# Kernel tuning notes

Measured on AMD Instinct MI355X. Metric: run time of the kernel, lower is better.

The kernel has to match this reference:

```python
import jax, jax.numpy as jnp
import numpy as np

B, L, C = 64, 2048, 20
H1, H2, F = 384, 16, 20


def _gru(x, h0, Wih, Whh, bih, bhh):
    """PyTorch-semantics GRU, batch_first. x:(B,L,I), h0:(B,H) -> (ys:(B,L,H), hT:(B,H))."""
    H = h0.shape[-1]
    # Precompute all input projections at once: (B, L, 3H)
    xp = jnp.einsum('bli,gi->blg', x, Wih) + bih

    def step(h, xp_t):
        gh = h @ Whh.T + bhh  # (B, 3H)
        r = jax.nn.sigmoid(xp_t[:, :H] + gh[:, :H])
        z = jax.nn.sigmoid(xp_t[:, H:2 * H] + gh[:, H:2 * H])
        n = jnp.tanh(xp_t[:, 2 * H:] + r * gh[:, 2 * H:])
        h_new = (1.0 - z) * n + z * h
        return h_new, h_new

    hT, ys = jax.lax.scan(step, h0, jnp.swapaxes(xp, 0, 1))
    return jnp.swapaxes(ys, 0, 1), hT


def _init_gru(key, I, H):
    k1, k2, k3, k4 = jax.random.split(key, 4)
    s = 1.0 / np.sqrt(H)
    return (jax.random.uniform(k1, (3 * H, I), minval=-s, maxval=s),
            jax.random.uniform(k2, (3 * H, H), minval=-s, maxval=s),
            jax.random.uniform(k3, (3 * H,), minval=-s, maxval=s),
            jax.random.uniform(k4, (3 * H,), minval=-s, maxval=s))


def setup_inputs() -> dict:
    key = jax.random.key(0)
    ks = jax.random.split(key, 6)
    x = jax.random.normal(ks[0], (B, L, C), dtype=jnp.float32)
    Wih1, Whh1, bih1, bhh1 = _init_gru(ks[1], C, H1)
    Wih2, Whh2, bih2, bhh2 = _init_gru(ks[2], H1, H2)
    Wih3, Whh3, bih3, bhh3 = _init_gru(ks[3], F, F)
    s = 1.0 / np.sqrt(H2)
    Wfc = jax.random.uniform(ks[4], (F, H2), minval=-s, maxval=s)
    bfc = jax.random.uniform(ks[5], (F,), minval=-s, maxval=s)
    return {
        'x': x,
        'h1': jnp.zeros((B, H1), jnp.float32),
        'h2': jnp.zeros((B, H2), jnp.float32),
        'h3': jnp.zeros((B, F), jnp.float32),
        'Wih1': Wih1, 'Whh1': Whh1, 'bih1': bih1, 'bhh1': bhh1,
        'Wih2': Wih2, 'Whh2': Whh2, 'bih2': bih2, 'bhh2': bhh2,
        'Wih3': Wih3, 'Whh3': Whh3, 'bih3': bih3, 'bhh3': bhh3,
        'Wfc': Wfc, 'bfc': bfc,
    }


def reference(x, h1, h2, h3,
              Wih1, Whh1, bih1, bhh1,
              Wih2, Whh2, bih2, bhh2,
              Wih3, Whh3, bih3, bhh3,
              Wfc, bfc):
    y1, h1f = _gru(x, h1, Wih1, Whh1, bih1, bhh1)          # (B, L, 384)
    y2, h2f = _gru(y1, h2, Wih2, Whh2, bih2, bhh2)         # (B, L, 16)
    y2 = jax.nn.relu(y2)
    # cat of two identical copies -> dual_fc -> sum over copy dim == 2 * tanh(fc)
    x_mid = 2.0 * jnp.tanh(jnp.einsum('blh,fh->blf', y2, Wfc) + bfc)  # (B, L, 20)
    y3, h3f = _gru(jnp.flip(x_mid, axis=1), h3, Wih3, Whh3, bih3, bhh3)
    x_out = jnp.tanh(y3)                                    # (B, L, 20)
    return (x_mid, x_out, h1f, h2f, h3f)
```

## Files before the change

### kernel.cpp

```cpp
#include <hip/hip_runtime.h>

typedef _Float16 f16x8 __attribute__((ext_vector_type(8)));
typedef _Float16 f16x2 __attribute__((ext_vector_type(2)));

union F16x8U { f16x8 v8; f16x2 v2[4]; };
union FP16U { _Float16 h; unsigned short u; };

__device__ __forceinline__ float dot2acc(f16x2 a, f16x2 b, float c) {
#if __has_builtin(__builtin_amdgcn_fdot2)
    return __builtin_amdgcn_fdot2(a, b, c, false);
#else
    return c + (float)a[0] * (float)b[0] + (float)a[1] * (float)b[1];
#endif
}

__device__ __forceinline__ float sigmoidf_(float x) {
    return __builtin_amdgcn_rcpf(1.f + __expf(-x));
}

__device__ __forceinline__ float tanhf_(float x) {
    float a = fabsf(x);
    float e = __expf(-2.f * a);
    float r = (1.f - e) * __builtin_amdgcn_rcpf(1.f + e);
    return copysignf(r, x);
}


__global__ void pack_weights(const float* __restrict__ Whh1,
                             const float* __restrict__ Wih1,
                             const float* __restrict__ Wih2,
                             _Float16* __restrict__ wsbase) {
    int tid = blockIdx.x * 256 + threadIdx.x;
    f16x8* whhp  = (f16x8*)wsbase;
    f16x8* wih1p = (f16x8*)(wsbase + 442368);
    _Float16* wih2h = wsbase + 470016;
    if (tid < 55296) {
        int c = tid % 18, thr = tid / 18;
        int g = c / 6, m = c % 6;
        int jl = thr % 96, ko = (thr / 96) % 8, q = thr / 768;
        int row = g * 384 + q * 96 + jl;
        int kb = ko * 48 + m * 8;
        f16x8 v;
#pragma unroll
        for (int i = 0; i < 8; ++i) v[i] = (_Float16)Whh1[row * 384 + kb + i];
        whhp[tid] = v;
    } else if (tid < 58752) {
        int t2 = tid - 55296;
        int m = t2 % 3, thr = t2 / 3;
        int jl = thr % 96, g = (thr / 96) % 3, q = thr / 288;
        int row = g * 384 + q * 96 + jl;
        f16x8 v;
#pragma unroll
        for (int i = 0; i < 8; ++i) {
            int kk = m * 8 + i;
            v[i] = (kk < 20) ? (_Float16)Wih1[row * 20 + kk] : (_Float16)0.f;
        }
        wih1p[t2] = v;
    } else if (tid < 77184) {
        int t3 = tid - 58752;
        wih2h[t3] = (_Float16)Wih2[t3];
    }
}

__global__ __launch_bounds__(768, 3) void gru1_scan(
    const float* __restrict__ x, const float* __restrict__ h1_0,
    const float* __restrict__ bih1, const float* __restrict__ bhh1,
    const f16x8* __restrict__ whhp, const f16x8* __restrict__ wih1p,
    const _Float16* __restrict__ wih2h,
    float* __restrict__ sxp2g, unsigned* __restrict__ exch,
    float* __restrict__ h1f_o) {
    const int bid = blockIdx.x;
    const int b = bid >> 2, q = bid & 3;
    const int tid = threadIdx.x;
    const int ko = tid / 96, jl = tid % 96;

    __shared__ __align__(16) _Float16 h1h[384];
    __shared__ __align__(16) _Float16 hhist[4][384];
    __shared__ __align__(16) _Float16 xsh[2][24];
    __shared__ __align__(16) float4 part4[8 * 96];
    __shared__ float part2[4 * 12 * 65];

    F16x8U W[18];
    {
        const f16x8* wp = whhp + ((size_t)((q * 8 + ko) * 96 + jl)) * 18;
#pragma unroll
        for (int c = 0; c < 18; ++c) W[c].v8 = wp[c];
    }
    F16x8U Wx[3];
    if (ko < 3) {
        const f16x8* wp = wih1p + ((size_t)((q * 3 + ko) * 96 + jl)) * 3;
#pragma unroll
        for (int c = 0; c < 3; ++c) Wx[c].v8 = wp[c];
    }

    float cbr = 0.f, cbz = 0.f, cxn = 0.f, chn = 0.f, hprev = 0.f;
    if (tid < 96) {
        int j = q * 96 + tid;
        cbr = bih1[j] + bhh1[j];
        cbz = bih1[384 + j] + bhh1[384 + j];
        cxn = bih1[768 + j];
        chn = bhh1[768 + j];
        hprev = h1_0[b * 384 + j];
    }
    if (tid < 384) h1h[tid] = (_Float16)h1_0[b * 384 + tid];
    const float* xb = x + (size_t)b * 40960;
    if (tid < 24) {
        xsh[0][tid] = (_Float16)((tid < 20) ? xb[tid] : 0.f);
        xsh[1][tid] = (_Float16)0.f;
    }

    unsigned* exb0 = exch + (size_t)b * 384;
    unsigned* exb1 = exch + 24576 + (size_t)b * 384;
    const int rs = tid - 384;
    const int gslot = (rs >= 0 && rs < 288) ? ((q * 96 + 96 + rs) % 384) : 0;

    const int o2 = tid >> 6, ks = tid & 63;
    const _Float16* w2row = wih2h + (q * 12 + o2) * 384 + ks * 6;

    __syncthreads();

    for (int t = 0; t < 2048; ++t) {
        float ar = 0.f, az = 0.f, ahn = 0.f, axn = 0.f;
        const _Float16* hbase = h1h + ko * 48;
#pragma unroll
        for (int m = 0; m < 6; ++m) {
            F16x8U hv; hv.v8 = *(const f16x8*)(hbase + m * 8);
#pragma unroll
            for (int i = 0; i < 4; ++i) {
                ar  = dot2acc(W[m].v2[i],      hv.v2[i], ar);
                az  = dot2acc(W[6 + m].v2[i],  hv.v2[i], az);
                ahn = dot2acc(W[12 + m].v2[i], hv.v2[i], ahn);
            }
        }
        if (ko < 3) {
            float acc = 0.f;
            const _Float16* xs = xsh[t & 1];
#pragma unroll
            for (int m = 0; m < 3; ++m) {
                F16x8U xv; xv.v8 = *(const f16x8*)(xs + m * 8);
#pragma unroll
                for (int i = 0; i < 4; ++i)
                    acc = dot2acc(Wx[m].v2[i], xv.v2[i], acc);
            }
            if (ko == 0) ar += acc;
            else if (ko == 1) az += acc;
            else axn += acc;
        }
        part4[ko * 96 + jl] = make_float4(ar, az, ahn, axn);
        __syncthreads();

        const unsigned tag = (unsigned)(t + 1);
        unsigned* exw = ((t + 1) & 1) ? exb1 : exb0;
        if (tid < 96) {
            float sr = cbr, sz = cbz, snh = chn, snx = cxn;
#pragma unroll
            for (int k = 0; k < 8; ++k) {
                float4 p = part4[k * 96 + tid];
                sr += p.x; sz += p.y; snh += p.z; snx += p.w;
            }
            float r = sigmoidf_(sr), z = sigmoidf_(sz);
            float n = tanhf_(snx + r * snh);
            hprev = (1.f - z) * n + z * hprev;
            FP16U hu; hu.h = (_Float16)hprev;
            __hip_atomic_store(&exw[q * 96 + tid], (tag << 16) | (unsigned)hu.u,
                               __ATOMIC_RELAXED, __HIP_MEMORY_SCOPE_AGENT);
            h1h[q * 96 + tid] = hu.h;
            hhist[t & 3][q * 96 + tid] = hu.h;
        }
        if (tid >= 96 && tid < 116 && t + 1 < 2048)
            xsh[(t + 1) & 1][tid - 96] = (_Float16)xb[(t + 1) * 20 + (tid - 96)];
        if (tid >= 384 && tid < 672) {
            unsigned w;
            do {
                w = __hip_atomic_load(&exw[gslot], __ATOMIC_RELAXED,
                                      __HIP_MEMORY_SCOPE_AGENT);
            } while ((w >> 16) != tag);
            FP16U hu; hu.u = (unsigned short)(w & 0xffffu);
            h1h[gslot] = hu.h;
            hhist[t & 3][gslot] = hu.h;
        }
        __syncthreads();

        if ((t & 3) == 3) {
            f16x2 w0 = *(const f16x2*)(w2row);
            f16x2 w1 = *(const f16x2*)(w2row + 2);
            f16x2 w2 = *(const f16x2*)(w2row + 4);
#pragma unroll
            for (int tq = 0; tq < 4; ++tq) {
                const _Float16* hrow = hhist[tq] + ks * 6;
                float a = dot2acc(w0, *(const f16x2*)hrow, 0.f);
                a = dot2acc(w1, *(const f16x2*)(hrow + 2), a);
                a = dot2acc(w2, *(const f16x2*)(hrow + 4), a);
                part2[(tq * 12 + o2) * 65 + ks] = a;
            }
            __syncthreads();
            if (tid < 48) {
                int tq = tid / 12, o = tid % 12;
                const float* pr = &part2[(tq * 12 + o) * 65];
                float s0 = 0.f, s1 = 0.f, s2 = 0.f, s3 = 0.f;
#pragma unroll
                for (int i2 = 0; i2 < 16; ++i2) {
                    s0 += pr[i2 * 4];     s1 += pr[i2 * 4 + 1];
                    s2 += pr[i2 * 4 + 2]; s3 += pr[i2 * 4 + 3];
                }
                __hip_atomic_store(
                    &sxp2g[((size_t)b * 2048 + (t - 3 + tq)) * 48 + q * 12 + o],
                    (s0 + s1) + (s2 + s3), __ATOMIC_RELAXED,
                    __HIP_MEMORY_SCOPE_AGENT);
            }
        }
    }
    if (tid < 96) h1f_o[b * 384 + q * 96 + tid] = hprev;
}

__global__ __launch_bounds__(64) void tail_scan(
    const float* __restrict__ sxp2g, const float* __restrict__ h2_0,
    const float* __restrict__ h3_0,
    const float* __restrict__ Whh2, const float* __restrict__ bih2,
    const float* __restrict__ bhh2,
    const float* __restrict__ Wfc, const float* __restrict__ bfc,
    const float* __restrict__ Wih3, const float* __restrict__ Whh3,
    const float* __restrict__ bih3, const float* __restrict__ bhh3,
    float* __restrict__ xmid, float* __restrict__ xout,
    float* __restrict__ h2f_o, float* __restrict__ h3f_o) {
    const int b = blockIdx.x;
    const int l = threadIdx.x;

    __shared__ __align__(16) float hs[32];

    float w2r[16]; float bx2 = 0.f, bh2 = 0.f;
    if (l < 48) {
#pragma unroll
        for (int k = 0; k < 16; ++k) w2r[k] = Whh2[l * 16 + k];
        bx2 = bih2[l]; bh2 = bhh2[l];
    }
    float wfc[16]; float bf = 0.f;
    if (l < 20) {
#pragma unroll
        for (int k = 0; k < 16; ++k) wfc[k] = Wfc[l * 16 + k];
        bf = bfc[l];
    }
    float h2all[16];
    {
        const float4* hp = (const float4*)(h2_0 + b * 16);
#pragma unroll
        for (int c = 0; c < 4; ++c) {
            float4 v = hp[c];
            h2all[c * 4 + 0] = v.x; h2all[c * 4 + 1] = v.y;
            h2all[c * 4 + 2] = v.z; h2all[c * 4 + 3] = v.w;
        }
    }
    float hown = (l < 16) ? h2_0[b * 16 + l] : 0.f;

    float* xm = xmid + (size_t)b * 40960;
    const float* sx = sxp2g + (size_t)b * 98304;

    float pre[8];
#pragma unroll
    for (int i = 0; i < 8; ++i) pre[i] = (l < 48) ? sx[i * 48 + l] : 0.f;

    for (int tg = 0; tg < 256; ++tg) {
#pragma unroll
        for (int tq = 0; tq < 8; ++tq) {
            const int t = tg * 8 + tq;
            float ax = pre[tq] + bx2;
            if (l < 48 && t + 8 < 2048) pre[tq] = sx[(size_t)(t + 8) * 48 + l];
            float a0 = 0.f, a1 = 0.f;
#pragma unroll
            for (int k = 0; k < 8; ++k) {
                a0 = __builtin_fmaf(h2all[k], w2r[k], a0);
                a1 = __builtin_fmaf(h2all[8 + k], w2r[8 + k], a1);
            }
            float ah = bh2 + a0 + a1;
            float s_   = ax + ah;
            float zpre = __shfl(s_, (16 + l) & 63);
            float xn3  = __shfl(ax, (32 + l) & 63);
            float ghn  = __shfl(ah, (32 + l) & 63);
            float r2 = sigmoidf_(s_);
            float z2 = sigmoidf_(zpre);
            float n2 = tanhf_(xn3 + r2 * ghn);
            float h2n = (1.f - z2) * n2 + z2 * hown;
            if (l < 16) { hown = h2n; hs[l] = h2n; }
            __builtin_amdgcn_wave_barrier();
            {
                const float4* hv = (const float4*)hs;
#pragma unroll
                for (int c = 0; c < 4; ++c) {
                    float4 v = hv[c];
                    h2all[c * 4 + 0] = v.x; h2all[c * 4 + 1] = v.y;
                    h2all[c * 4 + 2] = v.z; h2all[c * 4 + 3] = v.w;
                }
            }
            float f0 = 0.f, f1 = 0.f;
#pragma unroll
            for (int k = 0; k < 8; ++k) {
                f0 = __builtin_fmaf(fmaxf(h2all[k], 0.f), wfc[k], f0);
                f1 = __builtin_fmaf(fmaxf(h2all[8 + k], 0.f), wfc[8 + k], f1);
            }
            float a = bf + f0 + f1;
            if (l < 20) xm[t * 20 + l] = 2.f * tanhf_(a);
        }
    }
    if (l < 16) h2f_o[b * 16 + l] = hown;

    float wi3[20], wh3[20]; float bx3 = 0.f, bh3 = 0.f;
    if (l < 60) {
#pragma unroll
        for (int k = 0; k < 20; ++k) {
            wi3[k] = Wih3[l * 20 + k];
            wh3[k] = Whh3[l * 20 + k];
        }
        bx3 = bih3[l]; bh3 = bhh3[l];
    }
    float h3all[20];
    {
        const float4* hp = (const float4*)(h3_0 + b * 20);
#pragma unroll
        for (int c = 0; c < 5; ++c) {
            float4 v = hp[c];
            h3all[c * 4 + 0] = v.x; h3all[c * 4 + 1] = v.y;
            h3all[c * 4 + 2] = v.z; h3all[c * 4 + 3] = v.w;
        }
    }
    float h3own = (l < 20) ? h3_0[b * 20 + l] : 0.f;
    float* xo = xout + (size_t)b * 40960;

    float4 px[4][5];
#pragma unroll
    for (int i = 0; i < 4; ++i) {
        const float4* xr = (const float4*)(xm + (size_t)(2047 - i) * 20);
#pragma unroll
        for (int c = 0; c < 5; ++c) px[i][c] = xr[c];
    }

    for (int tg = 0; tg < 512; ++tg) {
#pragma unroll
        for (int tq = 0; tq < 4; ++tq) {
            const int t = 2047 - (tg * 4 + tq);
            float xv[20];
#pragma unroll
            for (int c = 0; c < 5; ++c) {
                float4 v = px[tq][c];
                xv[c * 4 + 0] = v.x; xv[c * 4 + 1] = v.y;
                xv[c * 4 + 2] = v.z; xv[c * 4 + 3] = v.w;
            }
            if (t - 4 >= 0) {
                const float4* xr = (const float4*)(xm + (size_t)(t - 4) * 20);
#pragma unroll
                for (int c = 0; c < 5; ++c) px[tq][c] = xr[c];
            }
            float x0 = 0.f, x1 = 0.f, g0 = 0.f, g1 = 0.f;
#pragma unroll
            for (int k = 0; k < 10; ++k) {
                x0 = __builtin_fmaf(xv[k], wi3[k], x0);
                x1 = __builtin_fmaf(xv[10 + k], wi3[10 + k], x1);
                g0 = __builtin_fmaf(h3all[k], wh3[k], g0);
                g1 = __builtin_fmaf(h3all[10 + k], wh3[10 + k], g1);
            }
            float ax = bx3 + x0 + x1;
            float ah = bh3 + g0 + g1;
            float s_   = ax + ah;
            float zpre = __shfl(s_, (20 + l) & 63);
            float xn_  = __shfl(ax, (40 + l) & 63);
            float ghn  = __shfl(ah, (40 + l) & 63);
            float r = sigmoidf_(s_);
            float z = sigmoidf_(zpre);
            float n = tanhf_(xn_ + r * ghn);
            float hn = (1.f - z) * n + z * h3own;
            if (l < 20) {
                h3own = hn;
                hs[l] = hn;
                xo[(size_t)(2047 - t) * 20 + l] = tanhf_(hn);
            }
            __builtin_amdgcn_wave_barrier();
#pragma unroll
            for (int c = 0; c < 5; ++c) {
                float4 v = ((const float4*)hs)[c];
                h3all[c * 4 + 0] = v.x; h3all[c * 4 + 1] = v.y;
                h3all[c * 4 + 2] = v.z; h3all[c * 4 + 3] = v.w;
            }
        }
    }
    if (l < 20) h3f_o[b * 20 + l] = h3own;
}

extern "C" void kernel_launch(void* const* d_in, const int* in_sizes, int n_in,
                              void* d_out, int out_size, void* d_ws, size_t ws_size,
                              hipStream_t stream) {
    const float* x    = (const float*)d_in[0];
    const float* h1   = (const float*)d_in[1];
    const float* h2   = (const float*)d_in[2];
    const float* h3   = (const float*)d_in[3];
    const float* Wih1 = (const float*)d_in[4];
    const float* Whh1 = (const float*)d_in[5];
    const float* bih1 = (const float*)d_in[6];
    const float* bhh1 = (const float*)d_in[7];
    const float* Wih2 = (const float*)d_in[8];
    const float* Whh2 = (const float*)d_in[9];
    const float* bih2 = (const float*)d_in[10];
    const float* bhh2 = (const float*)d_in[11];
    const float* Wih3 = (const float*)d_in[12];
    const float* Whh3 = (const float*)d_in[13];
    const float* bih3 = (const float*)d_in[14];
    const float* bhh3 = (const float*)d_in[15];
    const float* Wfc  = (const float*)d_in[16];
    const float* bfc  = (const float*)d_in[17];

    float* out  = (float*)d_out;
    float* xmid = out;
    float* xout = out + 2621440;
    float* h1f  = out + 5242880;
    float* h2f  = out + 5267456;
    float* h3f  = out + 5268480;

    char* ws = (char*)d_ws;
    _Float16* wsh  = (_Float16*)ws;
    float*    sxp2 = (float*)(ws + 1048576);
    unsigned* exch = (unsigned*)(ws + 26214400);

    hipMemsetAsync(exch, 0, 196608, stream);
    pack_weights<<<302, 256, 0, stream>>>(Whh1, Wih1, Wih2, wsh);
    gru1_scan<<<256, 768, 0, stream>>>(x, h1, bih1, bhh1,
                                       (const f16x8*)wsh,
                                       (const f16x8*)(wsh + 442368),
                                       wsh + 470016,
                                       sxp2, exch, h1f);
    tail_scan<<<64, 64, 0, stream>>>(sxp2, h2, h3,
                                     Whh2, bih2, bhh2, Wfc, bfc,
                                     Wih3, Whh3, bih3, bhh3,
                                     xmid, xout, h2f, h3f);
}
```

Baseline: 5.059 ms.

## Batch 16 sequences per block and compute GRU1 recurrence with MFMA

After: 8.240 ms. 1.63x slower.

```diff
diff --git a/kernel.cpp b/kernel.cpp
--- a/kernel.cpp
+++ b/kernel.cpp
@@ -1,18 +1,11 @@
 #include <hip/hip_runtime.h>
 
 typedef _Float16 f16x8 __attribute__((ext_vector_type(8)));
-typedef _Float16 f16x2 __attribute__((ext_vector_type(2)));
-
-union F16x8U { f16x8 v8; f16x2 v2[4]; };
+typedef _Float16 f16x4 __attribute__((ext_vector_type(4)));
+typedef float f32x4 __attribute__((ext_vector_type(4)));
+typedef unsigned long long u64_t;
+
 union FP16U { _Float16 h; unsigned short u; };
-
-__device__ __forceinline__ float dot2acc(f16x2 a, f16x2 b, float c) {
-#if __has_builtin(__builtin_amdgcn_fdot2)
-    return __builtin_amdgcn_fdot2(a, b, c, false);
-#else
-    return c + (float)a[0] * (float)b[0] + (float)a[1] * (float)b[1];
-#endif
-}
 
 __device__ __forceinline__ float sigmoidf_(float x) {
     return __builtin_amdgcn_rcpf(1.f + __expf(-x));
@@ -25,192 +18,258 @@
     return copysignf(r, x);
 }
 
+__device__ __forceinline__ f32x4 mfma16(f16x8 a, f16x8 b, f32x4 c) {
+    return __builtin_amdgcn_mfma_f32_16x16x32_f16(a, b, c, 0, 0, 0);
+}
+
 
 __global__ void pack_weights(const float* __restrict__ Whh1,
                              const float* __restrict__ Wih1,
                              const float* __restrict__ Wih2,
                              _Float16* __restrict__ wsbase) {
     int tid = blockIdx.x * 256 + threadIdx.x;
-    f16x8* whhp  = (f16x8*)wsbase;
-    f16x8* wih1p = (f16x8*)(wsbase + 442368);
-    _Float16* wih2h = wsbase + 470016;
-    if (tid < 55296) {
-        int c = tid % 18, thr = tid / 18;
-        int g = c / 6, m = c % 6;
-        int jl = thr % 96, ko = (thr / 96) % 8, q = thr / 768;
-        int row = g * 384 + q * 96 + jl;
-        int kb = ko * 48 + m * 8;
+    f16x8* whhA  = (f16x8*)wsbase;
+    f16x8* wih2f = (f16x8*)(wsbase + 491520);
+    if (tid < 61440) {
+        int l = tid & 63, fr = tid >> 6;
+        int fslot = fr % 20, w = fr / 20;
+        int kh = w & 1, jq = w >> 1;
+        int jc = jq % 6, q = jq / 6;
+        int tile, kt;
+        if (kh == 0) {
+            if (fslot < 7)       { tile = 0; kt = fslot; }
+            else if (fslot < 14) { tile = 1; kt = fslot - 7; }
+            else                 { tile = 2; kt = fslot - 14; }
+        } else {
+            if (fslot < 6)       { tile = 0; kt = 7 + fslot; }
+            else if (fslot < 12) { tile = 1; kt = 1 + fslot; }
+            else if (fslot < 18) { tile = 2; kt = fslot - 6; }
+            else if (fslot == 18){ tile = 3; kt = 12; }
+            else                 { tile = 4; kt = 0; }
+        }
+        int gate = (tile == 0) ? 0 : (tile == 1) ? 1 : 2;
+        int row = gate * 384 + q * 96 + jc * 16 + (l & 15);
+        int k0 = kt * 32 + (l >> 4) * 8;
         f16x8 v;
 #pragma unroll
-        for (int i = 0; i < 8; ++i) v[i] = (_Float16)Whh1[row * 384 + kb + i];
-        whhp[tid] = v;
-    } else if (tid < 58752) {
-        int t2 = tid - 55296;
-        int m = t2 % 3, thr = t2 / 3;
-        int jl = thr % 96, g = (thr / 96) % 3, q = thr / 288;
-        int row = g * 384 + q * 96 + jl;
+        for (int i = 0; i < 8; ++i) {
+            float f = 0.f;
+            if (tile != 4) {
+                int k = k0 + i;
+                if (tile == 3) {
+                    int kx = k - 384;
+                    f = (kx < 20) ? Wih1[row * 20 + kx] : 0.f;
+                } else if (k < 384) {
+                    f = Whh1[row * 384 + k];
+                } else if (tile < 2) {
+                    int kx = k - 384;
+                    f = (kx < 20) ? Wih1[row * 20 + kx] : 0.f;
+                }
+            }
+            v[i] = (_Float16)f;
+        }
+        whhA[tid] = v;
+    } else if (tid < 63744) {
+        int t2 = tid - 61440;
+        int l = t2 & 63, fi = t2 >> 6;
+        int q = fi / 9, vv = fi % 9;
+        int Mt = vv / 3, kk = 3 * q + vv % 3;
+        int row = Mt * 16 + (l & 15);
+        int k0 = kk * 32 + (l >> 4) * 8;
         f16x8 v;
 #pragma unroll
-        for (int i = 0; i < 8; ++i) {
-            int kk = m * 8 + i;
-            v[i] = (kk < 20) ? (_Float16)Wih1[row * 20 + kk] : (_Float16)0.f;
-        }
-        wih1p[t2] = v;
-    } else if (tid < 77184) {
-        int t3 = tid - 58752;
-        wih2h[t3] = (_Float16)Wih2[t3];
-    }
-}
-
-__global__ __launch_bounds__(768, 3) void gru1_scan(
+        for (int i = 0; i < 8; ++i) v[i] = (_Float16)Wih2[row * 384 + k0 + i];
+        wih2f[t2] = v;
+    }
+}
+
+__global__ __launch_bounds__(768) void gru1_scan(
     const float* __restrict__ x, const float* __restrict__ h1_0,
     const float* __restrict__ bih1, const float* __restrict__ bhh1,
-    const f16x8* __restrict__ whhp, const f16x8* __restrict__ wih1p,
-    const _Float16* __restrict__ wih2h,
-    float* __restrict__ sxp2g, unsigned* __restrict__ exch,
+    const f16x8* __restrict__ whhA, const f16x8* __restrict__ wih2f,
+    float* __restrict__ sxp2g, u64_t* __restrict__ exch,
     float* __restrict__ h1f_o) {
     const int bid = blockIdx.x;
-    const int b = bid >> 2, q = bid & 3;
+    const int g = bid >> 2, q = bid & 3;
     const int tid = threadIdx.x;
-    const int ko = tid / 96, jl = tid % 96;
-
-    __shared__ __align__(16) _Float16 h1h[384];
-    __shared__ __align__(16) _Float16 hhist[4][384];
-    __shared__ __align__(16) _Float16 xsh[2][24];
-    __shared__ __align__(16) float4 part4[8 * 96];
-    __shared__ float part2[4 * 12 * 65];
-
-    F16x8U W[18];
+    const int v = tid >> 6, l = tid & 63;
+    const int jc = v >> 1, kh = v & 1;
+    const int rg = l >> 4, b = l & 15;
+    const int j0 = q * 96 + jc * 16 + rg * 4;
+
+    __shared__ __align__(16) _Float16 hbuf[2][6784];
+    __shared__ __align__(16) float part[6528];
+
+    f16x8 A[20];
     {
-        const f16x8* wp = whhp + ((size_t)((q * 8 + ko) * 96 + jl)) * 18;
-#pragma unroll
-        for (int c = 0; c < 18; ++c) W[c].v8 = wp[c];
-    }
-    F16x8U Wx[3];
-    if (ko < 3) {
-        const f16x8* wp = wih1p + ((size_t)((q * 3 + ko) * 96 + jl)) * 3;
-#pragma unroll
-        for (int c = 0; c < 3; ++c) Wx[c].v8 = wp[c];
-    }
-
-    float cbr = 0.f, cbz = 0.f, cxn = 0.f, chn = 0.f, hprev = 0.f;
-    if (tid < 96) {
-        int j = q * 96 + tid;
-        cbr = bih1[j] + bhh1[j];
-        cbz = bih1[384 + j] + bhh1[384 + j];
-        cxn = bih1[768 + j];
-        chn = bhh1[768 + j];
-        hprev = h1_0[b * 384 + j];
-    }
-    if (tid < 384) h1h[tid] = (_Float16)h1_0[b * 384 + tid];
-    const float* xb = x + (size_t)b * 40960;
-    if (tid < 24) {
-        xsh[0][tid] = (_Float16)((tid < 20) ? xb[tid] : 0.f);
-        xsh[1][tid] = (_Float16)0.f;
-    }
-
-    unsigned* exb0 = exch + (size_t)b * 384;
-    unsigned* exb1 = exch + 24576 + (size_t)b * 384;
-    const int rs = tid - 384;
-    const int gslot = (rs >= 0 && rs < 288) ? ((q * 96 + 96 + rs) % 384) : 0;
-
-    const int o2 = tid >> 6, ks = tid & 63;
-    const _Float16* w2row = wih2h + (q * 12 + o2) * 384 + ks * 6;
-
+        const f16x8* ap = whhA + (size_t)(((q * 6 + jc) * 2 + kh) * 20) * 64 + l;
+#pragma unroll
+        for (int c = 0; c < 20; ++c) A[c] = ap[c * 64];
+    }
+    const bool xw = (v < 9);
+    const int ktx = 3 * q + v % 3, Mtx = v / 3;
+    f16x8 Ax;
+    if (xw) Ax = wih2f[(q * 9 + v) * 64 + l];
+
+    float bR[4], bZ[4], bXN[4], bHN[4], hp[4];
+    if (kh == 0) {
+#pragma unroll
+        for (int i = 0; i < 4; ++i) {
+            int j = j0 + i;
+            bR[i]  = bih1[j] + bhh1[j];
+            bZ[i]  = bih1[384 + j] + bhh1[384 + j];
+            bXN[i] = bih1[768 + j];
+            bHN[i] = bhh1[768 + j];
+            hp[i]  = h1_0[(size_t)(g * 16 + b) * 384 + j];
+        }
+    }
+
+    int wo[6], lo[6];
+    const int p = jc * 64 + l;
+    if (kh == 1) {
+#pragma unroll
+        for (int k = 0; k < 6; ++k) {
+            int idx = p + 384 * k;
+            int r_ = idx >> 4, b2 = idx & 15;
+            int jwr = (q * 48 + 48 + r_) % 192;
+            wo[k] = jwr * 16 + b2;
+            lo[k] = b2 * 424 + jwr * 2;
+        }
+    }
+    const int bx_ = p / 20, xi_ = p % 20;
+
+    for (int idx = tid; idx < 6784; idx += 768) {
+        int bb = idx / 424, k = idx % 424;
+        float val = 0.f;
+        if (k < 384) val = h1_0[(size_t)(g * 16 + bb) * 384 + k];
+        else if (k < 404) val = x[(size_t)(g * 16 + bb) * 40960 + (k - 384)];
+        hbuf[0][idx] = (_Float16)val;
+        hbuf[1][idx] = (_Float16)0.f;
+    }
+    u64_t* exg = exch + (size_t)g * 6144;
     __syncthreads();
 
     for (int t = 0; t < 2048; ++t) {
-        float ar = 0.f, az = 0.f, ahn = 0.f, axn = 0.f;
-        const _Float16* hbase = h1h + ko * 48;
-#pragma unroll
-        for (int m = 0; m < 6; ++m) {
-            F16x8U hv; hv.v8 = *(const f16x8*)(hbase + m * 8);
+        const int cur = t & 1, nxt = cur ^ 1;
+        const _Float16* hc = hbuf[cur];
+        _Float16* hn = hbuf[nxt];
+        const unsigned tag = (unsigned)(t + 1);
+        u64_t* exw = exg + ((t + 1) & 1) * 3072;
+
+        float xreg = 0.f;
+        if (kh == 1 && p < 320 && t + 1 < 2048)
+            xreg = x[(size_t)(g * 16 + bx_) * 40960 + (t + 1) * 20 + xi_];
+
+        f32x4 aR{0.f, 0.f, 0.f, 0.f}, aZ{0.f, 0.f, 0.f, 0.f};
+        f32x4 aN{0.f, 0.f, 0.f, 0.f}, aX{0.f, 0.f, 0.f, 0.f};
+        if (kh == 0) {
+#pragma unroll
+            for (int ki = 0; ki < 7; ++ki) {
+                f16x8 Bf = *(const f16x8*)(hc + b * 424 + ki * 32 + rg * 8);
+                aR = mfma16(A[ki], Bf, aR);
+                aZ = mfma16(A[7 + ki], Bf, aZ);
+                if (ki < 6) aN = mfma16(A[14 + ki], Bf, aN);
+            }
+        } else {
+#pragma unroll
+            for (int ki = 0; ki < 7; ++ki) {
+                f16x8 Bf = *(const f16x8*)(hc + b * 424 + (6 + ki) * 32 + rg * 8);
+                if (ki > 0) {
+                    aR = mfma16(A[ki - 1], Bf, aR);
+                    aZ = mfma16(A[5 + ki], Bf, aZ);
+                }
+                if (ki < 6) aN = mfma16(A[12 + ki], Bf, aN);
+                if (ki == 6) aX = mfma16(A[18], Bf, aX);
+            }
+        }
+
+        if (xw && t > 0) {
+            f16x8 Bx = *(const f16x8*)(hc + b * 424 + ktx * 32 + rg * 8);
+            f32x4 px = mfma16(Ax, Bx, (f32x4){0.f, 0.f, 0.f, 0.f});
+            float* dst = sxp2g + ((size_t)(g * 16 + b) * 2048 + (t - 1)) * 48 +
+                         Mtx * 16 + rg * 4;
+#pragma unroll
+            for (int i = 0; i < 4; ++i) atomicAdd(dst + i, px[i]);
+        }
+
+        if (kh == 1) {
+            float* pp = part + (jc * 64 + l) * 17;
 #pragma unroll
             for (int i = 0; i < 4; ++i) {
-                ar  = dot2acc(W[m].v2[i],      hv.v2[i], ar);
-                az  = dot2acc(W[6 + m].v2[i],  hv.v2[i], az);
-                ahn = dot2acc(W[12 + m].v2[i], hv.v2[i], ahn);
-            }
-        }
-        if (ko < 3) {
-            float acc = 0.f;
-            const _Float16* xs = xsh[t & 1];
-#pragma unroll
-            for (int m = 0; m < 3; ++m) {
-                F16x8U xv; xv.v8 = *(const f16x8*)(xs + m * 8);
-#pragma unroll
-                for (int i = 0; i < 4; ++i)
-                    acc = dot2acc(Wx[m].v2[i], xv.v2[i], acc);
-            }
-            if (ko == 0) ar += acc;
-            else if (ko == 1) az += acc;
-            else axn += acc;
-        }
-        part4[ko * 96 + jl] = make_float4(ar, az, ahn, axn);
+                pp[i] = aR[i]; pp[4 + i] = aZ[i];
+                pp[8 + i] = aN[i]; pp[12 + i] = aX[i];
+            }
+        }
         __syncthreads();
 
-        const unsigned tag = (unsigned)(t + 1);
-        unsigned* exw = ((t + 1) & 1) ? exb1 : exb0;
-        if (tid < 96) {
-            float sr = cbr, sz = cbz, snh = chn, snx = cxn;
-#pragma unroll
-            for (int k = 0; k < 8; ++k) {
-                float4 p = part4[k * 96 + tid];
-                sr += p.x; sz += p.y; snh += p.z; snx += p.w;
-            }
-            float r = sigmoidf_(sr), z = sigmoidf_(sz);
-            float n = tanhf_(snx + r * snh);
-            hprev = (1.f - z) * n + z * hprev;
-            FP16U hu; hu.h = (_Float16)hprev;
-            __hip_atomic_store(&exw[q * 96 + tid], (tag << 16) | (unsigned)hu.u,
-                               __ATOMIC_RELAXED, __HIP_MEMORY_SCOPE_AGENT);
-            h1h[q * 96 + tid] = hu.h;
-            hhist[t & 3][q * 96 + tid] = hu.h;
-        }
-        if (tid >= 96 && tid < 116 && t + 1 < 2048)
-            xsh[(t + 1) & 1][tid - 96] = (_Float16)xb[(t + 1) * 20 + (tid - 96)];
-        if (tid >= 384 && tid < 672) {
-            unsigned w;
+        if (kh == 0) {
+            const float* pp = part + (jc * 64 + l) * 17;
+            _Float16 hh[4];
+#pragma unroll
+            for (int i = 0; i < 4; ++i) {
+                float sR = aR[i] + pp[i];
+                float sZ = aZ[i] + pp[4 + i];
+                float sN = aN[i] + pp[8 + i];
+                float sX = aX[i] + pp[12 + i];
+                float r = sigmoidf_(sR + bR[i]);
+                float z = sigmoidf_(sZ + bZ[i]);
+                float n = tanhf_(sX + bXN[i] + r * (sN + bHN[i]));
+                float h = n + z * (hp[i] - n);
+                hp[i] = h;
+                hh[i] = (_Float16)h;
+            }
+            FP16U u0, u1, u2, u3;
+            u0.h = hh[0]; u1.h = hh[1]; u2.h = hh[2]; u3.h = hh[3];
+            unsigned w01 = (unsigned)u0.u | ((unsigned)u1.u << 16);
+            unsigned w23 = (unsigned)u2.u | ((unsigned)u3.u << 16);
+            u64_t e0 = (u64_t)w01 | ((u64_t)tag << 32);
+            u64_t e1 = (u64_t)w23 | ((u64_t)tag << 32);
+            int wA = (j0 >> 1) * 16 + b;
+            __hip_atomic_store(exw + wA, e0, __ATOMIC_RELAXED,
+                               __HIP_MEMORY_SCOPE_AGENT);
+            __hip_atomic_store(exw + wA + 16, e1, __ATOMIC_RELAXED,
+                               __HIP_MEMORY_SCOPE_AGENT);
+            f16x4 hq; hq[0] = hh[0]; hq[1] = hh[1]; hq[2] = hh[2]; hq[3] = hh[3];
+            *(f16x4*)(hn + b * 424 + j0) = hq;
+        } else {
+            if (p < 320 && t + 1 < 2048)
+                hn[bx_ * 424 + 384 + xi_] = (_Float16)xreg;
+            u64_t vv0, vv1, vv2, vv3, vv4, vv5;
+            bool ok;
             do {
-                w = __hip_atomic_load(&exw[gslot], __ATOMIC_RELAXED,
-                                      __HIP_MEMORY_SCOPE_AGENT);
-            } while ((w >> 16) != tag);
-            FP16U hu; hu.u = (unsigned short)(w & 0xffffu);
-            h1h[gslot] = hu.h;
-            hhist[t & 3][gslot] = hu.h;
+                vv0 = __hip_atomic_load(exw + wo[0], __ATOMIC_RELAXED, __HIP_MEMORY_SCOPE_AGENT);
+                vv1 = __hip_atomic_load(exw + wo[1], __ATOMIC_RELAXED, __HIP_MEMORY_SCOPE_AGENT);
+                vv2 = __hip_atomic_load(exw + wo[2], __ATOMIC_RELAXED, __HIP_MEMORY_SCOPE_AGENT);
+                vv3 = __hip_atomic_load(exw + wo[3], __ATOMIC_RELAXED, __HIP_MEMORY_SCOPE_AGENT);
+                vv4 = __hip_atomic_load(exw + wo[4], __ATOMIC_RELAXED, __HIP_MEMORY_SCOPE_AGENT);
+                vv5 = __hip_atomic_load(exw + wo[5], __ATOMIC_RELAXED, __HIP_MEMORY_SCOPE_AGENT);
+                ok = ((unsigned)(vv0 >> 32) == tag) & ((unsigned)(vv1 >> 32) == tag) &
+                     ((unsigned)(vv2 >> 32) == tag) & ((unsigned)(vv3 >> 32) == tag) &
+                     ((unsigned)(vv4 >> 32) == tag) & ((unsigned)(vv5 >> 32) == tag);
+            } while (!ok);
+            *(unsigned*)(hn + lo[0]) = (unsigned)vv0;
+            *(unsigned*)(hn + lo[1]) = (unsigned)vv1;
+            *(unsigned*)(hn + lo[2]) = (unsigned)vv2;
+            *(unsigned*)(hn + lo[3]) = (unsigned)vv3;
+            *(unsigned*)(hn + lo[4]) = (unsigned)vv4;
+            *(unsigned*)(hn + lo[5]) = (unsigned)vv5;
         }
         __syncthreads();
-
-        if ((t & 3) == 3) {
-            f16x2 w0 = *(const f16x2*)(w2row);
-            f16x2 w1 = *(const f16x2*)(w2row + 2);
-            f16x2 w2 = *(const f16x2*)(w2row + 4);
-#pragma unroll
-            for (int tq = 0; tq < 4; ++tq) {
-                const _Float16* hrow = hhist[tq] + ks * 6;
-                float a = dot2acc(w0, *(const f16x2*)hrow, 0.f);
-                a = dot2acc(w1, *(const f16x2*)(hrow + 2), a);
-                a = dot2acc(w2, *(const f16x2*)(hrow + 4), a);
-                part2[(tq * 12 + o2) * 65 + ks] = a;
-            }
-            __syncthreads();
-            if (tid < 48) {
-                int tq = tid / 12, o = tid % 12;
-                const float* pr = &part2[(tq * 12 + o) * 65];
-                float s0 = 0.f, s1 = 0.f, s2 = 0.f, s3 = 0.f;
-#pragma unroll
-                for (int i2 = 0; i2 < 16; ++i2) {
-                    s0 += pr[i2 * 4];     s1 += pr[i2 * 4 + 1];
-                    s2 += pr[i2 * 4 + 2]; s3 += pr[i2 * 4 + 3];
-                }
-                __hip_atomic_store(
-                    &sxp2g[((size_t)b * 2048 + (t - 3 + tq)) * 48 + q * 12 + o],
-                    (s0 + s1) + (s2 + s3), __ATOMIC_RELAXED,
-                    __HIP_MEMORY_SCOPE_AGENT);
-            }
-        }
-    }
-    if (tid < 96) h1f_o[b * 384 + q * 96 + tid] = hprev;
+    }
+
+    if (xw) {
+        const _Float16* hc = hbuf[0];
+        f16x8 Bx = *(const f16x8*)(hc + b * 424 + ktx * 32 + rg * 8);
+        f32x4 px = mfma16(Ax, Bx, (f32x4){0.f, 0.f, 0.f, 0.f});
+        float* dst = sxp2g + ((size_t)(g * 16 + b) * 2048 + 2047) * 48 +
+                     Mtx * 16 + rg * 4;
+#pragma unroll
+        for (int i = 0; i < 4; ++i) atomicAdd(dst + i, px[i]);
+    }
+    if (kh == 0) {
+        float4 hv = make_float4(hp[0], hp[1], hp[2], hp[3]);
+        *(float4*)(h1f_o + (size_t)(g * 16 + b) * 384 + j0) = hv;
+    }
 }
 
 __global__ __launch_bounds__(64) void tail_scan(
@@ -416,15 +475,15 @@
     char* ws = (char*)d_ws;
     _Float16* wsh  = (_Float16*)ws;
     float*    sxp2 = (float*)(ws + 1048576);
-    unsigned* exch = (unsigned*)(ws + 26214400);
+    u64_t*    exch = (u64_t*)(ws + 26214400);
 
     hipMemsetAsync(exch, 0, 196608, stream);
-    pack_weights<<<302, 256, 0, stream>>>(Whh1, Wih1, Wih2, wsh);
-    gru1_scan<<<256, 768, 0, stream>>>(x, h1, bih1, bhh1,
-                                       (const f16x8*)wsh,
-                                       (const f16x8*)(wsh + 442368),
-                                       wsh + 470016,
-                                       sxp2, exch, h1f);
+    hipMemsetAsync(sxp2, 0, 25165824, stream);
+    pack_weights<<<249, 256, 0, stream>>>(Whh1, Wih1, Wih2, wsh);
+    gru1_scan<<<16, 768, 0, stream>>>(x, h1, bih1, bhh1,
+                                      (const f16x8*)wsh,
+                                      (const f16x8*)(wsh + 491520),
+                                      sxp2, exch, h1f);
     tail_scan<<<64, 64, 0, stream>>>(sxp2, h2, h3,
                                      Whh2, bih2, bhh2, Wfc, bfc,
                                      Wih3, Whh3, bih3, bhh3,
```

## Overlap local-slice gate dot products with remote hidden-state exchange polling

Applied to the files above, without the earlier changes.

After: 4.997 ms. No clear change (-1.2%).

```diff
diff --git a/kernel.cpp b/kernel.cpp
--- a/kernel.cpp
+++ b/kernel.cpp
@@ -73,6 +73,7 @@
     const int b = bid >> 2, q = bid & 3;
     const int tid = threadIdx.x;
     const int ko = tid / 96, jl = tid % 96;
+    const int lq = ko >> 1;
 
     __shared__ __align__(16) _Float16 h1h[384];
     __shared__ __align__(16) _Float16 hhist[4][384];
@@ -108,18 +109,20 @@
         xsh[0][tid] = (_Float16)((tid < 20) ? xb[tid] : 0.f);
         xsh[1][tid] = (_Float16)0.f;
     }
+    float xreg = 0.f;
+    if (tid >= 96 && tid < 116) xreg = xb[20 + (tid - 96)];
 
     unsigned* exb0 = exch + (size_t)b * 384;
     unsigned* exb1 = exch + 24576 + (size_t)b * 384;
-    const int rs = tid - 384;
-    const int gslot = (rs >= 0 && rs < 288) ? ((q * 96 + 96 + rs) % 384) : 0;
+
+    const int rt = (tid < 192 * q) ? tid : tid - 192;
+    const bool isloc = (lq == q);
+    const int gslot = (!isloc && rt < 288) ? ((q * 96 + 96 + rt) % 384) : 0;
 
     const int o2 = tid >> 6, ks = tid & 63;
     const _Float16* w2row = wih2h + (q * 12 + o2) * 384 + ks * 6;
 
-    __syncthreads();
-
-    for (int t = 0; t < 2048; ++t) {
+    auto gate_dots = [&](int xpar) {
         float ar = 0.f, az = 0.f, ahn = 0.f, axn = 0.f;
         const _Float16* hbase = h1h + ko * 48;
 #pragma unroll
@@ -134,7 +137,7 @@
         }
         if (ko < 3) {
             float acc = 0.f;
-            const _Float16* xs = xsh[t & 1];
+            const _Float16* xs = xsh[xpar];
 #pragma unroll
             for (int m = 0; m < 3; ++m) {
                 F16x8U xv; xv.v8 = *(const f16x8*)(xs + m * 8);
@@ -147,10 +150,16 @@
             else axn += acc;
         }
         part4[ko * 96 + jl] = make_float4(ar, az, ahn, axn);
-        __syncthreads();
-
+    };
+
+    __syncthreads();
+    gate_dots(0);
+    __syncthreads();
+
+    for (int t = 0; t < 2048; ++t) {
         const unsigned tag = (unsigned)(t + 1);
         unsigned* exw = ((t + 1) & 1) ? exb1 : exb0;
+
         if (tid < 96) {
             float sr = cbr, sz = cbz, snh = chn, snx = cxn;
 #pragma unroll
@@ -166,10 +175,15 @@
                                __ATOMIC_RELAXED, __HIP_MEMORY_SCOPE_AGENT);
             h1h[q * 96 + tid] = hu.h;
             hhist[t & 3][q * 96 + tid] = hu.h;
-        }
-        if (tid >= 96 && tid < 116 && t + 1 < 2048)
-            xsh[(t + 1) & 1][tid - 96] = (_Float16)xb[(t + 1) * 20 + (tid - 96)];
-        if (tid >= 384 && tid < 672) {
+        } else if (tid < 116) {
+            xsh[(t + 1) & 1][tid - 96] = (_Float16)xreg;
+            if (t + 2 < 2048) xreg = xb[(t + 2) * 20 + (tid - 96)];
+        }
+        __syncthreads();
+
+        if (isloc) {
+            gate_dots((t + 1) & 1);
+        } else if (rt < 288) {
             unsigned w;
             do {
                 w = __hip_atomic_load(&exw[gslot], __ATOMIC_RELAXED,
@@ -181,6 +195,8 @@
         }
         __syncthreads();
 
+        if (!isloc) gate_dots((t + 1) & 1);
+
         if ((t & 3) == 3) {
             f16x2 w0 = *(const f16x2*)(w2row);
             f16x2 w1 = *(const f16x2*)(w2row + 2);
@@ -203,12 +219,11 @@
                     s0 += pr[i2 * 4];     s1 += pr[i2 * 4 + 1];
                     s2 += pr[i2 * 4 + 2]; s3 += pr[i2 * 4 + 3];
                 }
-                __hip_atomic_store(
-                    &sxp2g[((size_t)b * 2048 + (t - 3 + tq)) * 48 + q * 12 + o],
-                    (s0 + s1) + (s2 + s3), __ATOMIC_RELAXED,
-                    __HIP_MEMORY_SCOPE_AGENT);
-            }
-        }
+                sxp2g[((size_t)b * 2048 + (t - 3 + tq)) * 48 + q * 12 + o] =
+                    (s0 + s1) + (s2 + s3);
+            }
+        }
+        __syncthreads();
     }
     if (tid < 96) h1f_o[b * 384 + q * 96 + tid] = hprev;
 }
```
